# Optimization experiments

Measured on AMD Instinct MI355X. Metric: run time of the kernel, lower is better.

Reference implementation:

```python
import jax, jax.numpy as jnp
import numpy as np
from jax.scipy.special import erf, erfinv

SQRT2 = 1.4142135623730951
COST_CLASS, COST_BBOX, COST_GIOU = 1.0, 1.0, 1.0
NORM_MU, NORM_SIGMA = -5.5, 2.5        # torch.distributions.Normal(-5.5, 2.5)
HALFNORM_SCALE = 0.3                   # torch.distributions.HalfNormal(0.3)
LOOKAHEAD = 2


def box_cxcywh_to_xyxy(b):
    cx, cy, w, h = jnp.split(b, 4, axis=-1)
    return jnp.concatenate([cx - 0.5 * w, cy - 0.5 * h, cx + 0.5 * w, cy + 0.5 * h], axis=-1)


def generalized_box_iou(boxes1, boxes2):
    # boxes1 [M,4], boxes2 [N,4] in xyxy -> [M,N]
    area1 = (boxes1[:, 2] - boxes1[:, 0]) * (boxes1[:, 3] - boxes1[:, 1])
    area2 = (boxes2[:, 2] - boxes2[:, 0]) * (boxes2[:, 3] - boxes2[:, 1])
    lt = jnp.maximum(boxes1[:, None, :2], boxes2[None, :, :2])
    rb = jnp.minimum(boxes1[:, None, 2:], boxes2[None, :, 2:])
    wh = jnp.clip(rb - lt, 0.0)
    inter = wh[..., 0] * wh[..., 1]
    union = area1[:, None] + area2[None, :] - inter
    iou = inter / union
    lt2 = jnp.minimum(boxes1[:, None, :2], boxes2[None, :, :2])
    rb2 = jnp.maximum(boxes1[:, None, 2:], boxes2[None, :, 2:])
    wh2 = jnp.clip(rb2 - lt2, 0.0)
    area = wh2[..., 0] * wh2[..., 1]
    return iou - (area - union) / area


def build_fx_T(pred_logits, pred_boxes, tgt_boxes, tgt_labels, T):
    bs, Q, _ = pred_logits.shape
    N = tgt_labels.shape[0]  # bs * T
    out_prob = jax.nn.softmax(pred_logits.reshape(bs * Q, -1), axis=-1)
    out_bbox = pred_boxes.reshape(bs * Q, 4)
    cost_class = -out_prob[:, tgt_labels]                                       # [bs*Q, N]
    cost_bbox = jnp.sum(jnp.abs(out_bbox[:, None, :] - tgt_boxes[None, :, :]), axis=-1)  # L1 cdist
    cost_giou = -generalized_box_iou(box_cxcywh_to_xyxy(out_bbox), box_cxcywh_to_xyxy(tgt_boxes))
    C = COST_BBOX * cost_bbox + COST_CLASS * cost_class + COST_GIOU * cost_giou
    C = C.reshape(bs, Q, N)
    # permute(0,2,1) then block-diag boolean select: keep only same-batch target rows
    Cp = jnp.transpose(C, (0, 2, 1)).reshape(bs, bs, T, Q)
    Csel = Cp[jnp.arange(bs), jnp.arange(bs)].reshape(N, Q)                     # [N, Q]
    # prob = Normal(mu, sigma).cdf(-C); fx = HalfNormal(scale).icdf(prob)  (elementwise)
    prob = 0.5 * (1.0 + erf((-Csel - NORM_MU) / (NORM_SIGMA * SQRT2)))
    fx = HALFNORM_SCALE * SQRT2 * erfinv(prob)
    return fx.T                                                                 # [Q, N]


def batch_my_linear_sum_assignment(B, row_lookups):
    # B: [Q, N] float cost, row_lookups: [N, N] int block-diagonal 0/1 matrix.
    N = row_lookups.shape[-1]

    def step(B, _):
        # topk(clamp(B, max=100), 2, dim=0).values -> diff along dim 0 -> second_best - best
        top2 = jax.lax.top_k(jnp.minimum(B, 100.0).T, LOOKAHEAD)[0]   # [N, 2]
        delta = top2[:, 1] - top2[:, 0]                               # torch.diff(values, n=1, dim=0)
        col = jnp.argmax(jnp.abs(delta))
        row = jnp.argmax(B[:, col])
        B = B.at[:, col].set(0.0)
        # torch: B[row, row_lookups[col]] = 0  -- long 0/1 values used as COLUMN INDICES (faithful)
        B = B.at[row, row_lookups[col]].set(0.0)
        B = B.at[row, col].set(-1e-07)
        return B, None

    B, _ = jax.lax.scan(step, B, None, length=N)
    return B < 0


def setup_inputs() -> dict:
    key = jax.random.key(0)
    k1, k2, k3, k4 = jax.random.split(key, 4)
    bs, Q, num_classes, T = 32, 512, 92, 24
    N = bs * T
    return {
        "pred_logits": jax.random.normal(k1, (bs, Q, num_classes), dtype=jnp.float32),
        "pred_boxes": jax.random.uniform(k2, (bs, Q, 4), dtype=jnp.float32),
        "tgt_boxes": jax.random.uniform(k3, (N, 4), dtype=jnp.float32),
        "tgt_labels": jax.random.randint(k4, (N,), 0, num_classes),
        "num_targets_per_image": T,
    }


def reference(pred_logits, pred_boxes, tgt_boxes, tgt_labels, num_targets_per_image):
    bs = pred_logits.shape[0]
    T = int(num_targets_per_image)
    N = bs * T
    fx_T = build_fx_T(pred_logits, pred_boxes, tgt_boxes, tgt_labels, T)        # [Q, N]
    # lookup_sizes_vfast with uniform sizes: block-diagonal ones matrix [N, N]
    row_lookups = jnp.kron(jnp.eye(bs, dtype=jnp.int32), jnp.ones((T, T), dtype=jnp.int32))
    return batch_my_linear_sum_assignment(fx_T, row_lookups)                    # bool [Q, N]
```

## Files before the change

kernel.cpp:

```cpp
#include <hip/hip_runtime.h>
#include <math.h>

#pragma clang fp contract(off)

#define QN   512
#define NN   768
#define BSZ  32
#define TPI  24
#define NCLS 92
#define SROWS 64

#define WFENCE() asm volatile("s_waitcnt lgkmcnt(0)" ::: "memory")


__device__ __forceinline__ float xla_erf_f32(float x) {
#pragma clang fp contract(off)
  float x2 = x * x;
  float p = -2.72614225801306e-10f;
  p = fmaf(x2, p, 2.77068142495902e-08f);
  p = fmaf(x2, p, -2.10102402082508e-06f);
  p = fmaf(x2, p, -5.69250639462346e-05f);
  p = fmaf(x2, p, -7.34990630326855e-04f);
  p = fmaf(x2, p, -2.95459980854025e-03f);
  p = fmaf(x2, p, -1.60960333262415e-02f);
  p = x * p;
  float q = -1.45660718464996e-05f;
  q = fmaf(x2, q, -2.13374055278905e-04f);
  q = fmaf(x2, q, -1.68282697438203e-03f);
  q = fmaf(x2, q, -7.37332916720468e-03f);
  q = fmaf(x2, q, -1.42647390514189e-02f);
  float r = p / q;
  if (fabsf(x) >= 3.832506856900711f) r = copysignf(1.0f, x);
  return r;
}

__device__ __forceinline__ float xla_erfinv_f32(float b) {
#pragma clang fp contract(off)
  float bb = b * b;
  float u = (-bb) + 1.0f;
  float w = -((float)log((double)u));
  float p;
  if (w < 5.0f) {
    float ww = w - 2.5f;
    p = 2.81022636e-08f;
    p = p * ww + 3.43273939e-07f;
    p = p * ww - 3.5233877e-06f;
    p = p * ww - 4.39150654e-06f;
    p = p * ww + 0.00021858087f;
    p = p * ww - 0.00125372503f;
    p = p * ww - 0.00417768164f;
    p = p * ww + 0.246640727f;
    p = p * ww + 1.50140941f;
  } else {
    float ww = (float)sqrt((double)w) - 3.0f;
    p = -0.000200214257f;
    p = p * ww + 0.000100950558f;
    p = p * ww + 0.00134934322f;
    p = p * ww - 0.00367342844f;
    p = p * ww + 0.00573950773f;
    p = p * ww - 0.0076224613f;
    p = p * ww + 0.00943887047f;
    p = p * ww + 1.00167406f;
    p = p * ww + 2.83297682f;
  }
  return p * b;
}


__global__ void __launch_bounds__(256) k_softmax_stats(const float* __restrict__ logits,
                                                       float* __restrict__ mx,
                                                       float* __restrict__ sm) {
#pragma clang fp contract(off)
  __shared__ float buf[SROWS][NCLS + 1];
  int r0 = blockIdx.x * SROWS;
  const float* src = logits + (size_t)r0 * NCLS;
  for (int i = threadIdx.x; i < SROWS * NCLS; i += 256) {
    int rr = i / NCLS, cc = i - rr * NCLS;
    buf[rr][cc] = src[i];
  }
  __syncthreads();
  int r = threadIdx.x;
  if (r < SROWS) {
    const float* row = buf[r];
    float m = -INFINITY;
    for (int j = 0; j < NCLS; ++j) m = fmaxf(m, row[j]);
    float s = 0.0f;
    for (int j = 0; j < NCLS; ++j) s += expf(row[j] - m);
    mx[r0 + r] = m;
    sm[r0 + r] = s;
  }
}


__device__ __forceinline__ float fx_rest(float pc, const float* __restrict__ pboxes,
                                         float4 tb, int r) {
#pragma clang fp contract(off)
  float cost_class = -pc;

  float4 pb = ((const float4*)pboxes)[r];

  float cost_bbox = ((fabsf(pb.x - tb.x) + fabsf(pb.y - tb.y)) +
                     fabsf(pb.z - tb.z)) + fabsf(pb.w - tb.w);

  float p0 = pb.x - 0.5f * pb.z;
  float p1 = pb.y - 0.5f * pb.w;
  float p2 = pb.x + 0.5f * pb.z;
  float p3 = pb.y + 0.5f * pb.w;
  float t0 = tb.x - 0.5f * tb.z;
  float t1 = tb.y - 0.5f * tb.w;
  float t2 = tb.x + 0.5f * tb.z;
  float t3 = tb.y + 0.5f * tb.w;

  float area1 = (p2 - p0) * (p3 - p1);
  float area2 = (t2 - t0) * (t3 - t1);
  float ltx = fmaxf(p0, t0), lty = fmaxf(p1, t1);
  float rbx = fminf(p2, t2), rby = fminf(p3, t3);
  float whx = fmaxf(rbx - ltx, 0.0f), why = fmaxf(rby - lty, 0.0f);
  float inter = whx * why;
  float uni = (area1 + area2) - inter;
  float iou = inter / uni;
  float l2x = fminf(p0, t0), l2y = fminf(p1, t1);
  float r2x = fmaxf(p2, t2), r2y = fmaxf(p3, t3);
  float w2x = fmaxf(r2x - l2x, 0.0f), w2y = fmaxf(r2y - l2y, 0.0f);
  float area = w2x * w2y;
  float giou = iou - (area - uni) / area;

  float C = (cost_bbox + cost_class) + (-giou);

  float z = (-C + 5.5f) / 3.5355339059327378f;
  float prob = 0.5f * (1.0f + xla_erf_f32(z));
  return 0.4242640687119285f * xla_erfinv_f32(prob);
}


__global__ void __launch_bounds__(256) k_buildkey(const float* __restrict__ logits,
                                                  const float* __restrict__ pboxes,
                                                  const float* __restrict__ tboxes,
                                                  const int* __restrict__ tlabels,
                                                  const float* __restrict__ mx,
                                                  const float* __restrict__ sm,
                                                  float* __restrict__ B01,
                                                  unsigned long long* __restrict__ skey_g) {
#pragma clang fp contract(off)
  __shared__ float w1s[4], w2s[4], wbs[4];
  __shared__ int   wis[4];
  const int n = blockIdx.x;
  const int tid = threadIdx.x, lane = tid & 63, wave = tid >> 6;
  const int lab = tlabels[n];
  const float4 tb = ((const float4*)tboxes)[n];
  const int rbase = (n / TPI) * QN;

  float f[2];
#pragma unroll
  for (int k = 0; k < 2; ++k) {
    int q = tid + 256 * k;
    int r = rbase + q;
    float pc = expf(logits[(size_t)r * NCLS + lab] - mx[r]) / sm[r];
    f[k] = fx_rest(pc, pboxes, tb, r);
    if (n < 2) B01[n * QN + q] = f[k];
  }

  float c0 = fminf(f[0], 100.0f), c1f = fminf(f[1], 100.0f);
  float v1 = fmaxf(c0, c1f), v2 = fminf(c0, c1f);
  float bv; int bi;
  if (f[1] > f[0]) { bv = f[1]; bi = tid + 256; } else { bv = f[0]; bi = tid; }
  for (int off = 32; off > 0; off >>= 1) {
    float o1 = __shfl_xor(v1, off), o2 = __shfl_xor(v2, off);
    float ov = __shfl_xor(bv, off); int oi = __shfl_xor(bi, off);
    if (o1 > v1) { v2 = fmaxf(v1, o2); v1 = o1; }
    else v2 = fmaxf(v2, o1);
    if (ov > bv || (ov == bv && oi < bi)) { bv = ov; bi = oi; }
  }
  if (lane == 0) { w1s[wave] = v1; w2s[wave] = v2; wbs[wave] = bv; wis[wave] = bi; }
  __syncthreads();
  if (tid == 0) {
    float V1 = w1s[0], V2 = w2s[0], BV = wbs[0]; int BI = wis[0];
    for (int w = 1; w < 4; ++w) {
      float o1 = w1s[w], o2 = w2s[w];
      if (o1 > V1) { V2 = fmaxf(V1, o2); V1 = o1; }
      else V2 = fmaxf(V2, o1);
      float ov = wbs[w]; int oi = wis[w];
      if (ov > BV || (ov == BV && oi < BI)) { BV = ov; BI = oi; }
    }
    unsigned long long key = 0ull;
    if (n >= 2) {
      unsigned vb = __float_as_uint(V1 - V2);
      key = ((unsigned long long)vb << 32) |
            (unsigned long long)(((unsigned)(1023 - n) << 16) | (unsigned)BI);
    }
    skey_g[n] = key;
  }
}


__device__ __forceinline__ void wave_maxcount(const float* arr, int lane, float bound,
                                              float& mxv, int& cnt) {
  float m = -INFINITY; int c = 0;
#pragma unroll
  for (int k = 0; k < QN / 64; ++k) {
    float v = fminf(arr[lane + 64 * k], 100.0f);
    if (v < bound) {
      if (v > m) { m = v; c = 1; }
      else if (v == m) c++;
    }
  }
  for (int off = 32; off > 0; off >>= 1) {
    float om = __shfl_xor(m, off);
    int oc = __shfl_xor(c, off);
    if (om > m) { m = om; c = oc; }
    else if (om == m) c += oc;
  }
  mxv = m; cnt = c;
}

__device__ __forceinline__ int wave_argmax(const float* arr, int lane) {
  float bv = -INFINITY; int bi = 0x7fffffff;
#pragma unroll
  for (int k = 0; k < QN / 64; ++k) {
    float v = arr[lane + 64 * k];
    if (v > bv) { bv = v; bi = lane + 64 * k; }
  }
  for (int off = 32; off > 0; off >>= 1) {
    float ov = __shfl_xor(bv, off);
    int oi = __shfl_xor(bi, off);
    if (ov > bv || (ov == bv && oi < bi)) { bv = ov; bi = oi; }
  }
  return bi;
}

__device__ __forceinline__ bool ms_update(float x, float& a1, int& c1, float& a2, int& c2) {
  x = fminf(x, 100.0f);
  bool rescan = false;
  if (x == a1) {
    if (--c1 == 0) rescan = true;
  } else if (x == a2) {
    if (--c2 == 0) rescan = true;
  }
  if (!rescan) {
    if (0.0f > a1) { a2 = a1; c2 = c1; a1 = 0.0f; c1 = 1; }
    else if (0.0f == a1) c1++;
    else if (0.0f > a2) { a2 = 0.0f; c2 = 1; }
    else if (0.0f == a2) c2++;
  }
  return rescan;
}


__global__ void __launch_bounds__(512) k_scan(const float* __restrict__ B01,
                                              const unsigned long long* __restrict__ skey_g,
                                              int* __restrict__ asg_out) {
  __shared__ unsigned long long skey[1024];
  __shared__ unsigned long long spay[1024];
  __shared__ float m0[QN];
  __shared__ float m1[QN];
  __shared__ int   asg[NN];
  __shared__ int   minpos[QN];
  __shared__ float fst[4];
  __shared__ int   ist[4];
  const int tid  = threadIdx.x;
  const int lane = tid & 63;
  const int wave = tid >> 6;

  for (int i = tid; i < QN; i += 512) {
    m0[i] = B01[i];
    m1[i] = B01[QN + i];
    minpos[i] = 0x7fffffff;
  }
  for (int i = tid; i < NN; i += 512) { asg[i] = -1; skey[i] = skey_g[i]; }
  for (int i = NN + tid; i < 1024; i += 512) skey[i] = 0ull;
  __syncthreads();

  for (int kk2 = 2; kk2 <= 1024; kk2 <<= 1) {
    for (int j = kk2 >> 1; j > 0; j >>= 1) {
      int g = tid;
      int t = ((g & ~(j - 1)) << 1) | (g & (j - 1));
      int l = t | j;
      unsigned long long a = skey[t], b = skey[l];
      bool sw = ((t & kk2) == 0) ? (a < b) : (a > b);
      if (sw) { skey[t] = b; skey[l] = a; }
      __syncthreads();
    }
  }

#pragma unroll
  for (int k = 0; k < 2; ++k) {
    int pp = tid + 512 * k;
    unsigned long long key = skey[pp];
    int r = (int)(key & 0x1FF);
    spay[pp] = (unsigned long long)__float_as_uint(fminf(m0[r], 100.0f)) |
               ((unsigned long long)__float_as_uint(fminf(m1[r], 100.0f)) << 32);
    if (key != 0ull) atomicMin(&minpos[r], pp);
  }
  __syncthreads();
#pragma unroll
  for (int k = 0; k < 2; ++k) {
    int pp = tid + 512 * k;
    unsigned long long key = skey[pp];
    int r = (int)(key & 0x1FF);
    if (key != 0ull && minpos[r] == pp) skey[pp] |= 0x8000ull;
  }
  if (wave == 0) {
    float A1, A2; int C1, C2;
    wave_maxcount(m0, lane, INFINITY, A1, C1);
    wave_maxcount(m0, lane, A1, A2, C2);
    if (lane == 0) { fst[0] = A1; fst[1] = A2; ist[0] = C1; ist[1] = C2; }
  } else if (wave == 1) {
    float B1, B2; int D1, D2;
    wave_maxcount(m1, lane, INFINITY, B1, D1);
    wave_maxcount(m1, lane, B1, B2, D2);
    if (lane == 0) { fst[2] = B1; fst[3] = B2; ist[2] = D1; ist[3] = D2; }
  }
  __syncthreads();
  if (wave != 0) return;

  float a1 = fst[0], a2 = fst[1], b1 = fst[2], b2 = fst[3];
  int   c1 = ist[0], c2 = ist[1], d1 = ist[2], d2 = ist[3];

  int p = 0, it = 0, w0 = -64;
  float cv = 0.0f, ix0 = 0.0f, ix1 = 0.0f;
  unsigned lo = 0; int row = 0; bool ft = false;
  int negpos0 = -1, negpos1 = -1, dt_m0 = -1, dt_m1 = -1;
  bool trivial0 = false, trivial1 = false;
  int asg0 = -1, asg1 = -1;

  while (it < NN) {
    if (p >= w0 + 64) {
      w0 = p & ~63;
      unsigned long long kk = skey[w0 + lane];
      unsigned long long yy = spay[w0 + lane];
      cv  = __uint_as_float((unsigned)(kk >> 32));
      lo  = (unsigned)kk;
      row = (int)(lo & 0x1FF);
      ft  = (lo & 0x8000u) != 0;
      ix0 = __uint_as_float((unsigned)yy);
      ix1 = __uint_as_float((unsigned)(yy >> 32));
    }
    float gap0 = (c1 >= 2) ? 0.0f : (a1 - a2);
    float gap1 = (d1 >= 2) ? 0.0f : (b1 - b2);
    float best = fmaxf(gap0, gap1);

    float x0 = trivial0 ? ((row == negpos0) ? -1e-07f : 0.0f)
                        : ((ft && row != dt_m0) ? ix0 : 0.0f);
    float x1 = trivial1 ? ((row == negpos1) ? -1e-07f : 0.0f)
                        : ((ft && row != dt_m1) ? ix1 : 0.0f);
    bool slow = ((!trivial0) && !(a1 > 0.0f && a2 > 0.0f)) ||
                ((!trivial1) && !(b1 > 0.0f && b2 > 0.0f));
    bool ev = slow ||
              (trivial0 ? (x0 != 0.0f) : (x0 == a1 || x0 == a2)) ||
              (trivial1 ? (x1 != 0.0f) : (x1 == b1 || x1 == b2));
    bool sel = !(cv > best);

    int base = p - w0;
    unsigned long long valid = ~0ull << base;
    unsigned long long selm = __ballot(sel) & valid;
    unsigned long long evm  = __ballot(ev)  & valid;
    int lsel = selm ? (int)__builtin_ctzll(selm) : 64;
    int lev  = evm  ? (int)__builtin_ctzll(evm)  : 64;
    int lmin = (lsel < lev) ? lsel : lev;
    int pref = lmin - base;
    int rem = NN - it;
    if (pref > rem) pref = rem;

    if ((int)lane >= base && (int)lane < base + pref) {
      m0[row] = 0.0f;
      m1[row] = 0.0f;
      asg[1023 - (int)(lo >> 16)] = row;
    }
    p += pref; it += pref;
    if (it >= NN) break;
    if (lmin == 64) continue;

    WFENCE();
    if (lsel <= lev) {
      int col = (gap1 > gap0) ? 1 : 0;
      if (col == 0) {
        int rw = trivial0 ? ((negpos0 == 0) ? 1 : 0) : wave_argmax(m0, lane);
        float x1p = m1[rw];
#pragma unroll
        for (int k = 0; k < QN / 64; ++k) m0[lane + 64 * k] = 0.0f;
        if (lane == 0) { m0[rw] = -1e-07f; m1[rw] = 0.0f; }
        WFENCE();
        a1 = 0.0f; c1 = QN - 1; a2 = -1e-07f; c2 = 1;
        trivial0 = true; negpos0 = rw;
        dt_m1 = rw;
        if (negpos1 == rw) negpos1 = -1;
        if (ms_update(x1p, b1, d1, b2, d2)) {
          WFENCE();
          wave_maxcount(m1, lane, INFINITY, b1, d1);
          wave_maxcount(m1, lane, b1, b2, d2);
        }
        asg0 = rw;
        if (asg1 == rw) asg1 = -1;
      } else {
        int rw = trivial1 ? ((negpos1 == 0) ? 1 : 0) : wave_argmax(m1, lane);
        float x0p = m0[rw];
#pragma unroll
        for (int k = 0; k < QN / 64; ++k) m1[lane + 64 * k] = 0.0f;
        if (lane == 0) { m1[rw] = -1e-07f; m0[rw] = 0.0f; }
        WFENCE();
        b1 = 0.0f; d1 = QN - 1; b2 = -1e-07f; d2 = 1;
        trivial1 = true; negpos1 = rw;
        dt_m0 = rw;
        if (negpos0 == rw) negpos0 = -1;
        if (ms_update(x0p, a1, c1, a2, c2)) {
          WFENCE();
          wave_maxcount(m0, lane, INFINITY, a1, c1);
          wave_maxcount(m0, lane, a1, a2, c2);
        }
        asg1 = rw;
        if (asg0 == rw) asg0 = -1;
      }
      ++it;
    } else {
      float cx0 = __shfl(x0, lmin);
      float cx1 = __shfl(x1, lmin);
      int crow  = __shfl(row, lmin);
      int ccol  = 1023 - __shfl((int)(lo >> 16), lmin);
      if (lane == 0) { m0[crow] = 0.0f; m1[crow] = 0.0f; asg[ccol] = crow; }
      if (negpos0 == crow) negpos0 = -1;
      if (negpos1 == crow) negpos1 = -1;
      if (ms_update(cx0, a1, c1, a2, c2)) {
        WFENCE();
        wave_maxcount(m0, lane, INFINITY, a1, c1);
        wave_maxcount(m0, lane, a1, a2, c2);
      }
      if (ms_update(cx1, b1, d1, b2, d2)) {
        WFENCE();
        wave_maxcount(m1, lane, INFINITY, b1, d1);
        wave_maxcount(m1, lane, b1, b2, d2);
      }
      if (asg0 == crow) asg0 = -1;
      if (asg1 == crow) asg1 = -1;
      ++p; ++it;
    }
  }

  if (lane == 0) { asg[0] = asg0; asg[1] = asg1; }
  WFENCE();
#pragma unroll
  for (int k = 0; k < NN / 64; ++k) {
    int i = lane + 64 * k;
    asg_out[i] = asg[i];
  }
}


__global__ void k_out(const int* __restrict__ asg, int* __restrict__ out, int total) {
  int t = blockIdx.x * blockDim.x + threadIdx.x;
  if (t >= total) return;
  int q = t / NN;
  int n = t - q * NN;
  out[t] = (asg[n] == q) ? 1 : 0;
}

extern "C" void kernel_launch(void* const* d_in, const int* in_sizes, int n_in,
                              void* d_out, int out_size, void* d_ws, size_t ws_size,
                              hipStream_t stream) {
  const float* logits  = (const float*)d_in[0];
  const float* pboxes  = (const float*)d_in[1];
  const float* tboxes  = (const float*)d_in[2];
  const int*   tlabels = (const int*)d_in[3];

  float* mx = (float*)d_ws;
  float* sm = mx + BSZ * QN;
  float* B01 = sm + BSZ * QN;
  unsigned long long* skey_g = (unsigned long long*)(B01 + 1024);
  int* asg_g = (int*)(skey_g + NN);
  int* out = (int*)d_out;

  hipLaunchKernelGGL(k_softmax_stats, dim3((BSZ * QN) / SROWS), dim3(256), 0, stream,
                     logits, mx, sm);
  hipLaunchKernelGGL(k_buildkey, dim3(NN), dim3(256), 0, stream,
                     logits, pboxes, tboxes, tlabels, mx, sm, B01, skey_g);
  hipLaunchKernelGGL(k_scan, dim3(1), dim3(512), 0, stream, B01, skey_g, asg_g);
  hipLaunchKernelGGL(k_out, dim3((QN * NN) / 256), dim3(256), 0, stream,
                     asg_g, out, QN * NN);
}
```

Before: 49.94 us.

## Sort keys in registers via wave shuffles and fuse top-2 max-count scans

The shared-memory bitonic sort, which needed a block-wide barrier at every stage, is split up. Stages with stride 64 or less now run in registers: each lane holds two keys and exchanges them with partners through 64-bit xor shuffles. Only strides of 128 and above still go through shared memory with __syncthreads. Separately, the two-pass max/second-max count over a column is merged into one pass that tracks the top two values and their counts, with a matching butterfly merge. This halves the shared-memory reads on rescans in the serial loop, at the cost of more register compare logic and a harder tie-handling merge.

```diff
diff --git a/kernel.cpp b/kernel.cpp
--- a/kernel.cpp
+++ b/kernel.cpp
@@ -193,24 +193,35 @@
 }
 
 
-__device__ __forceinline__ void wave_maxcount(const float* arr, int lane, float bound,
-                                              float& mxv, int& cnt) {
-  float m = -INFINITY; int c = 0;
+__device__ __forceinline__ void wave_top2count(const float* arr, int lane,
+                                               float& a1o, int& c1o, float& a2o, int& c2o) {
+  float m1 = -INFINITY, m2 = -INFINITY; int k1 = 0, k2 = 0;
 #pragma unroll
   for (int k = 0; k < QN / 64; ++k) {
     float v = fminf(arr[lane + 64 * k], 100.0f);
-    if (v < bound) {
-      if (v > m) { m = v; c = 1; }
-      else if (v == m) c++;
-    }
+    if (v > m1) { m2 = m1; k2 = k1; m1 = v; k1 = 1; }
+    else if (v == m1) k1++;
+    else if (v > m2) { m2 = v; k2 = 1; }
+    else if (v == m2) k2++;
   }
   for (int off = 32; off > 0; off >>= 1) {
-    float om = __shfl_xor(m, off);
-    int oc = __shfl_xor(c, off);
-    if (om > m) { m = om; c = oc; }
-    else if (om == m) c += oc;
-  }
-  mxv = m; cnt = c;
+    float om1 = __shfl_xor(m1, off), om2 = __shfl_xor(m2, off);
+    int ok1 = __shfl_xor(k1, off), ok2 = __shfl_xor(k2, off);
+    if (om1 == m1) {
+      k1 += ok1;
+      if (om2 == m2) k2 += ok2;
+      else if (om2 > m2) { m2 = om2; k2 = ok2; }
+    } else if (om1 > m1) {
+      if (om2 > m1) { m2 = om2; k2 = ok2; }
+      else if (om2 == m1) { m2 = m1; k2 = k1 + ok2; }
+      else { m2 = m1; k2 = k1; }
+      m1 = om1; k1 = ok1;
+    } else {
+      if (om1 > m2) { m2 = om1; k2 = ok1; }
+      else if (om1 == m2) k2 += ok1;
+    }
+  }
+  a1o = m1; c1o = k1; a2o = m2; c2o = k2;
 }
 
 __device__ __forceinline__ int wave_argmax(const float* arr, int lane) {
@@ -243,6 +254,31 @@
     else if (0.0f == a2) c2++;
   }
   return rescan;
+}
+
+__device__ __forceinline__ unsigned long long shflx64(unsigned long long v, int m) {
+  unsigned lo = (unsigned)v, hi = (unsigned)(v >> 32);
+  lo = __shfl_xor(lo, m); hi = __shfl_xor(hi, m);
+  return ((unsigned long long)hi << 32) | lo;
+}
+
+__device__ __forceinline__ void reg_stage(unsigned long long& v0, unsigned long long& v1,
+                                          int lane, int e0, int j, int kk2) {
+  if (j == 64) {
+    bool desc = ((e0 & kk2) == 0);
+    unsigned long long hi = v0 > v1 ? v0 : v1;
+    unsigned long long lo = v0 > v1 ? v1 : v0;
+    v0 = desc ? hi : lo;
+    v1 = desc ? lo : hi;
+  } else {
+    unsigned long long p0 = shflx64(v0, j);
+    unsigned long long p1 = shflx64(v1, j);
+    bool tside = (lane & j) == 0;
+    bool km0 = (((e0 & kk2) == 0) == tside);
+    bool km1 = ((((e0 + 64) & kk2) == 0) == tside);
+    v0 = km0 ? (v0 > p0 ? v0 : p0) : (v0 < p0 ? v0 : p0);
+    v1 = km1 ? (v1 > p1 ? v1 : p1) : (v1 < p1 ? v1 : p1);
+  }
 }
 
 
@@ -270,14 +306,28 @@
   for (int i = NN + tid; i < 1024; i += 512) skey[i] = 0ull;
   __syncthreads();
 
-  for (int kk2 = 2; kk2 <= 1024; kk2 <<= 1) {
-    for (int j = kk2 >> 1; j > 0; j >>= 1) {
-      int g = tid;
-      int t = ((g & ~(j - 1)) << 1) | (g & (j - 1));
-      int l = t | j;
-      unsigned long long a = skey[t], b = skey[l];
-      bool sw = ((t & kk2) == 0) ? (a < b) : (a > b);
-      if (sw) { skey[t] = b; skey[l] = a; }
+  {
+    const int e0 = wave * 128 + lane;
+    unsigned long long v0 = skey[e0], v1 = skey[e0 + 64];
+    for (int kk2 = 2; kk2 <= 128; kk2 <<= 1)
+      for (int j = kk2 >> 1; j > 0; j >>= 1)
+        reg_stage(v0, v1, lane, e0, j, kk2);
+    skey[e0] = v0; skey[e0 + 64] = v1;
+    __syncthreads();
+
+    for (int kk2 = 256; kk2 <= 1024; kk2 <<= 1) {
+      for (int j = kk2 >> 1; j >= 128; j >>= 1) {
+        int t = ((tid & ~(j - 1)) << 1) | (tid & (j - 1));
+        int l = t | j;
+        unsigned long long a = skey[t], b = skey[l];
+        bool sw = ((t & kk2) == 0) ? (a < b) : (a > b);
+        if (sw) { skey[t] = b; skey[l] = a; }
+        __syncthreads();
+      }
+      v0 = skey[e0]; v1 = skey[e0 + 64];
+      for (int j = 64; j > 0; j >>= 1)
+        reg_stage(v0, v1, lane, e0, j, kk2);
+      skey[e0] = v0; skey[e0 + 64] = v1;
       __syncthreads();
     }
   }
@@ -301,13 +351,11 @@
   }
   if (wave == 0) {
     float A1, A2; int C1, C2;
-    wave_maxcount(m0, lane, INFINITY, A1, C1);
-    wave_maxcount(m0, lane, A1, A2, C2);
+    wave_top2count(m0, lane, A1, C1, A2, C2);
     if (lane == 0) { fst[0] = A1; fst[1] = A2; ist[0] = C1; ist[1] = C2; }
   } else if (wave == 1) {
     float B1, B2; int D1, D2;
-    wave_maxcount(m1, lane, INFINITY, B1, D1);
-    wave_maxcount(m1, lane, B1, B2, D2);
+    wave_top2count(m1, lane, B1, D1, B2, D2);
     if (lane == 0) { fst[2] = B1; fst[3] = B2; ist[2] = D1; ist[3] = D2; }
   }
   __syncthreads();
@@ -386,8 +434,7 @@
         if (negpos1 == rw) negpos1 = -1;
         if (ms_update(x1p, b1, d1, b2, d2)) {
           WFENCE();
-          wave_maxcount(m1, lane, INFINITY, b1, d1);
-          wave_maxcount(m1, lane, b1, b2, d2);
+          wave_top2count(m1, lane, b1, d1, b2, d2);
         }
         asg0 = rw;
         if (asg1 == rw) asg1 = -1;
@@ -404,8 +451,7 @@
         if (negpos0 == rw) negpos0 = -1;
         if (ms_update(x0p, a1, c1, a2, c2)) {
           WFENCE();
-          wave_maxcount(m0, lane, INFINITY, a1, c1);
-          wave_maxcount(m0, lane, a1, a2, c2);
+          wave_top2count(m0, lane, a1, c1, a2, c2);
         }
         asg1 = rw;
         if (asg0 == rw) asg0 = -1;
@@ -421,13 +467,11 @@
       if (negpos1 == crow) negpos1 = -1;
       if (ms_update(cx0, a1, c1, a2, c2)) {
         WFENCE();
-        wave_maxcount(m0, lane, INFINITY, a1, c1);
-        wave_maxcount(m0, lane, a1, a2, c2);
+        wave_top2count(m0, lane, a1, c1, a2, c2);
       }
       if (ms_update(cx1, b1, d1, b2, d2)) {
         WFENCE();
-        wave_maxcount(m1, lane, INFINITY, b1, d1);
-        wave_maxcount(m1, lane, b1, b2, d2);
+        wave_top2count(m1, lane, b1, d1, b2, d2);
       }
       if (asg0 == crow) asg0 = -1;
       if (asg1 == crow) asg1 = -1;
```

Result: slower. 51.75 us (+3.6%).

## Fuse softmax stats into cost build with per-slice partial top-2 reductions

Applied to the files above, without the earlier changes.

Merges the softmax-statistics kernel and the per-target cost/key kernel into one kernel. Each block loads 64 query rows of logits into shared memory, computes max and sum there, then evaluates fx for all 24 targets of its image. Each wave writes a partial top-2/argmax record per target and slice, and the single-block scan kernel merges the 8 slices before sorting. This removes a kernel launch, the global round trip for mx/sm, and the scattered per-target logit gathers. In exchange, the serial scan kernel gains extra merge work and partial-record reads.

```diff
diff --git a/kernel.cpp b/kernel.cpp
--- a/kernel.cpp
+++ b/kernel.cpp
@@ -8,7 +8,6 @@
 #define BSZ  32
 #define TPI  24
 #define NCLS 92
-#define SROWS 64
 
 #define WFENCE() asm volatile("s_waitcnt lgkmcnt(0)" ::: "memory")
 
@@ -67,37 +66,9 @@
 }
 
 
-__global__ void __launch_bounds__(256) k_softmax_stats(const float* __restrict__ logits,
-                                                       float* __restrict__ mx,
-                                                       float* __restrict__ sm) {
-#pragma clang fp contract(off)
-  __shared__ float buf[SROWS][NCLS + 1];
-  int r0 = blockIdx.x * SROWS;
-  const float* src = logits + (size_t)r0 * NCLS;
-  for (int i = threadIdx.x; i < SROWS * NCLS; i += 256) {
-    int rr = i / NCLS, cc = i - rr * NCLS;
-    buf[rr][cc] = src[i];
-  }
-  __syncthreads();
-  int r = threadIdx.x;
-  if (r < SROWS) {
-    const float* row = buf[r];
-    float m = -INFINITY;
-    for (int j = 0; j < NCLS; ++j) m = fmaxf(m, row[j]);
-    float s = 0.0f;
-    for (int j = 0; j < NCLS; ++j) s += expf(row[j] - m);
-    mx[r0 + r] = m;
-    sm[r0 + r] = s;
-  }
-}
-
-
-__device__ __forceinline__ float fx_rest(float pc, const float* __restrict__ pboxes,
-                                         float4 tb, int r) {
+__device__ __forceinline__ float fx_rest(float pc, float4 pb, float4 tb) {
 #pragma clang fp contract(off)
   float cost_class = -pc;
-
-  float4 pb = ((const float4*)pboxes)[r];
 
   float cost_bbox = ((fabsf(pb.x - tb.x) + fabsf(pb.y - tb.y)) +
                      fabsf(pb.z - tb.z)) + fabsf(pb.w - tb.w);
@@ -133,62 +104,61 @@
 }
 
 
-__global__ void __launch_bounds__(256) k_buildkey(const float* __restrict__ logits,
-                                                  const float* __restrict__ pboxes,
-                                                  const float* __restrict__ tboxes,
-                                                  const int* __restrict__ tlabels,
-                                                  const float* __restrict__ mx,
-                                                  const float* __restrict__ sm,
-                                                  float* __restrict__ B01,
-                                                  unsigned long long* __restrict__ skey_g) {
+__global__ void __launch_bounds__(256) k_stats_build(const float* __restrict__ logits,
+                                                     const float* __restrict__ pboxes,
+                                                     const float* __restrict__ tboxes,
+                                                     const int* __restrict__ tlabels,
+                                                     float* __restrict__ B01,
+                                                     float4* __restrict__ partial) {
 #pragma clang fp contract(off)
-  __shared__ float w1s[4], w2s[4], wbs[4];
-  __shared__ int   wis[4];
-  const int n = blockIdx.x;
+  __shared__ float buf[64][NCLS + 1];
+  __shared__ float mx_l[64], sm_l[64];
+  const int blk = blockIdx.x;
   const int tid = threadIdx.x, lane = tid & 63, wave = tid >> 6;
-  const int lab = tlabels[n];
-  const float4 tb = ((const float4*)tboxes)[n];
-  const int rbase = (n / TPI) * QN;
-
-  float f[2];
-#pragma unroll
-  for (int k = 0; k < 2; ++k) {
-    int q = tid + 256 * k;
-    int r = rbase + q;
-    float pc = expf(logits[(size_t)r * NCLS + lab] - mx[r]) / sm[r];
-    f[k] = fx_rest(pc, pboxes, tb, r);
-    if (n < 2) B01[n * QN + q] = f[k];
-  }
-
-  float c0 = fminf(f[0], 100.0f), c1f = fminf(f[1], 100.0f);
-  float v1 = fmaxf(c0, c1f), v2 = fminf(c0, c1f);
-  float bv; int bi;
-  if (f[1] > f[0]) { bv = f[1]; bi = tid + 256; } else { bv = f[0]; bi = tid; }
-  for (int off = 32; off > 0; off >>= 1) {
-    float o1 = __shfl_xor(v1, off), o2 = __shfl_xor(v2, off);
-    float ov = __shfl_xor(bv, off); int oi = __shfl_xor(bi, off);
-    if (o1 > v1) { v2 = fmaxf(v1, o2); v1 = o1; }
-    else v2 = fmaxf(v2, o1);
-    if (ov > bv || (ov == bv && oi < bi)) { bv = ov; bi = oi; }
-  }
-  if (lane == 0) { w1s[wave] = v1; w2s[wave] = v2; wbs[wave] = bv; wis[wave] = bi; }
+  const int r0 = blk * 64;
+  const int b = blk >> 3, slice = blk & 7;
+
+  const float* src = logits + (size_t)r0 * NCLS;
+  for (int i = tid; i < 64 * NCLS; i += 256) {
+    int rr = i / NCLS, cc = i - rr * NCLS;
+    buf[rr][cc] = src[i];
+  }
   __syncthreads();
-  if (tid == 0) {
-    float V1 = w1s[0], V2 = w2s[0], BV = wbs[0]; int BI = wis[0];
-    for (int w = 1; w < 4; ++w) {
-      float o1 = w1s[w], o2 = w2s[w];
-      if (o1 > V1) { V2 = fmaxf(V1, o2); V1 = o1; }
-      else V2 = fmaxf(V2, o1);
-      float ov = wbs[w]; int oi = wis[w];
-      if (ov > BV || (ov == BV && oi < BI)) { BV = ov; BI = oi; }
-    }
-    unsigned long long key = 0ull;
-    if (n >= 2) {
-      unsigned vb = __float_as_uint(V1 - V2);
-      key = ((unsigned long long)vb << 32) |
-            (unsigned long long)(((unsigned)(1023 - n) << 16) | (unsigned)BI);
-    }
-    skey_g[n] = key;
+  if (tid < 64) {
+    const float* row = buf[tid];
+    float m = -INFINITY;
+    for (int j = 0; j < NCLS; ++j) m = fmaxf(m, row[j]);
+    float s = 0.0f;
+    for (int j = 0; j < NCLS; ++j) s += expf(row[j] - m);
+    mx_l[tid] = m;
+    sm_l[tid] = s;
+  }
+  __syncthreads();
+
+  const int r = r0 + lane;
+  const float4 pb = ((const float4*)pboxes)[r];
+  const float m = mx_l[lane], s = sm_l[lane];
+
+#pragma unroll
+  for (int k = 0; k < 6; ++k) {
+    int nl = wave + 4 * k;
+    int n = b * TPI + nl;
+    int lab = tlabels[n];
+    float4 tb = ((const float4*)tboxes)[n];
+    float pc = expf(buf[lane][lab] - m) / s;
+    float fx = fx_rest(pc, pb, tb);
+    if (n < 2) B01[n * QN + r] = fx;
+
+    float v1 = fminf(fx, 100.0f), v2 = -INFINITY;
+    float bv = fx; int bi = r;
+    for (int off = 32; off > 0; off >>= 1) {
+      float o1 = __shfl_xor(v1, off), o2 = __shfl_xor(v2, off);
+      float ov = __shfl_xor(bv, off); int oi = __shfl_xor(bi, off);
+      if (o1 > v1) { v2 = fmaxf(v1, o2); v1 = o1; }
+      else v2 = fmaxf(v2, o1);
+      if (ov > bv || (ov == bv && oi < bi)) { bv = ov; bi = oi; }
+    }
+    if (lane == 0) partial[n * 8 + slice] = make_float4(v1, v2, bv, __int_as_float(bi));
   }
 }
 
@@ -247,7 +217,7 @@
 
 
 __global__ void __launch_bounds__(512) k_scan(const float* __restrict__ B01,
-                                              const unsigned long long* __restrict__ skey_g,
+                                              const float4* __restrict__ partial,
                                               int* __restrict__ asg_out) {
   __shared__ unsigned long long skey[1024];
   __shared__ unsigned long long spay[1024];
@@ -266,7 +236,26 @@
     m1[i] = B01[QN + i];
     minpos[i] = 0x7fffffff;
   }
-  for (int i = tid; i < NN; i += 512) { asg[i] = -1; skey[i] = skey_g[i]; }
+  for (int i = tid; i < NN; i += 512) {
+    asg[i] = -1;
+    float4 p0 = partial[i * 8];
+    float V1 = p0.x, V2 = p0.y, BV = p0.z; int BI = __float_as_int(p0.w);
+#pragma unroll
+    for (int sl = 1; sl < 8; ++sl) {
+      float4 pp = partial[i * 8 + sl];
+      if (pp.x > V1) { V2 = fmaxf(V1, pp.y); V1 = pp.x; }
+      else V2 = fmaxf(V2, pp.x);
+      float ov = pp.z; int oi = __float_as_int(pp.w);
+      if (ov > BV || (ov == BV && oi < BI)) { BV = ov; BI = oi; }
+    }
+    unsigned long long key = 0ull;
+    if (i >= 2) {
+      unsigned vb = __float_as_uint(V1 - V2);
+      key = ((unsigned long long)vb << 32) |
+            (unsigned long long)(((unsigned)(1023 - i) << 16) | (unsigned)BI);
+    }
+    skey[i] = key;
+  }
   for (int i = NN + tid; i < 1024; i += 512) skey[i] = 0ull;
   __syncthreads();
 
@@ -461,18 +450,14 @@
   const float* tboxes  = (const float*)d_in[2];
   const int*   tlabels = (const int*)d_in[3];
 
-  float* mx = (float*)d_ws;
-  float* sm = mx + BSZ * QN;
-  float* B01 = sm + BSZ * QN;
-  unsigned long long* skey_g = (unsigned long long*)(B01 + 1024);
-  int* asg_g = (int*)(skey_g + NN);
+  float* B01 = (float*)d_ws;
+  float4* partial = (float4*)(B01 + 1024);
+  int* asg_g = (int*)(partial + NN * 8);
   int* out = (int*)d_out;
 
-  hipLaunchKernelGGL(k_softmax_stats, dim3((BSZ * QN) / SROWS), dim3(256), 0, stream,
-                     logits, mx, sm);
-  hipLaunchKernelGGL(k_buildkey, dim3(NN), dim3(256), 0, stream,
-                     logits, pboxes, tboxes, tlabels, mx, sm, B01, skey_g);
-  hipLaunchKernelGGL(k_scan, dim3(1), dim3(512), 0, stream, B01, skey_g, asg_g);
+  hipLaunchKernelGGL(k_stats_build, dim3(BSZ * QN / 64), dim3(256), 0, stream,
+                     logits, pboxes, tboxes, tlabels, B01, partial);
+  hipLaunchKernelGGL(k_scan, dim3(1), dim3(512), 0, stream, B01, partial, asg_g);
   hipLaunchKernelGGL(k_out, dim3((QN * NN) / 256), dim3(256), 0, stream,
                      asg_g, out, QN * NN);
 }
```

Measured after the change: 56.13 us. +12.4%, slower.
